# Optimization experiments

Hardware: AMD Instinct MI355X
Metric: run time of the kernel (lower is better)

The kernel has to match this reference:

```python
import jax, jax.numpy as jnp
import numpy as np
import math

D_MODEL = 2048
B, S, PAST = 4, 2048, 2048


def setup_inputs() -> dict:
    key = jax.random.key(0)
    ks = jax.random.split(key, 8)
    scale = 0.02
    x = jax.random.normal(ks[0], (B, S, D_MODEL), dtype=jnp.float32)
    past_k = jax.random.normal(ks[1], (B, PAST, D_MODEL), dtype=jnp.float32)
    past_v = jax.random.normal(ks[2], (B, PAST, D_MODEL), dtype=jnp.float32)
    Wq = jax.random.normal(ks[3], (D_MODEL, D_MODEL), dtype=jnp.float32) * scale
    Wk = jax.random.normal(ks[4], (D_MODEL, D_MODEL), dtype=jnp.float32) * scale
    Wv = jax.random.normal(ks[5], (D_MODEL, D_MODEL), dtype=jnp.float32) * scale
    Wo = jax.random.normal(ks[6], (D_MODEL, D_MODEL), dtype=jnp.float32) * scale
    bq = jnp.zeros((D_MODEL,), jnp.float32)
    bk = jnp.zeros((D_MODEL,), jnp.float32)
    bv = jnp.zeros((D_MODEL,), jnp.float32)
    bo = jnp.zeros((D_MODEL,), jnp.float32)
    return {"x": x, "past_k": past_k, "past_v": past_v,
            "Wq": Wq, "bq": bq, "Wk": Wk, "bk": bk,
            "Wv": Wv, "bv": bv, "Wo": Wo, "bo": bo}


def reference(x, past_k, past_v, Wq, bq, Wk, bk, Wv, bv, Wo, bo):
    d_model = x.shape[-1]
    # torch Linear: y = x @ W.T + b; here W is stored [out, in] equivalently square
    q = jnp.einsum('bsd,ed->bse', x, Wq) + bq
    k = jnp.einsum('bsd,ed->bse', x, Wk) + bk
    v = jnp.einsum('bsd,ed->bse', x, Wv) + bv
    k_cache = jnp.concatenate([past_k, k], axis=1)  # [B, PAST+S, D]
    v_cache = jnp.concatenate([past_v, v], axis=1)
    scores = jnp.einsum('bqd,bkd->bqk', q, k_cache) / math.sqrt(d_model)
    weights = jax.nn.softmax(scores, axis=-1)
    attn = jnp.einsum('bqk,bkd->bqd', weights, v_cache)
    out = jnp.einsum('bqd,ed->bqe', attn, Wo) + bo
    return out, (k_cache, v_cache)
```

## Files before the change

### kernel.cpp

```cpp
#include <hip/hip_runtime.h>
#include <math.h>

typedef unsigned short u16;
typedef __bf16 bf16x8 __attribute__((ext_vector_type(8)));
typedef float f32x4 __attribute__((ext_vector_type(4)));
typedef float f32x16 __attribute__((ext_vector_type(16)));
typedef short s16x8 __attribute__((ext_vector_type(8)));

#define DM 2048
#define NB 4
#define SEQ 2048
#define PAST_N 2048
#define CS 4096

__device__ __forceinline__ u16 f2bf(float f) {
  unsigned u = __float_as_uint(f);
  u += 0x7fff + ((u >> 16) & 1);
  return (u16)(u >> 16);
}
__device__ __forceinline__ float bf2f(u16 h) {
  return __uint_as_float(((unsigned)h) << 16);
}

__device__ __forceinline__ void gl_lds16(const u16* g, u16* l) {
  __builtin_amdgcn_global_load_lds(
      (const __attribute__((address_space(1))) unsigned*)g,
      (__attribute__((address_space(3))) unsigned*)l, 16, 0, 0);
}

__device__ __forceinline__ bf16x8 ldsfrag32(const u16* s, int row, int ks, int hk) {
  const int byte_off = (row * 128 + ks * 32 + hk * 16) ^ ((row & 7) << 4);
  return *(const bf16x8*)((const char*)s + byte_off);
}

__device__ __forceinline__ void stage4(const u16* __restrict__ g, int ld,
                                       u16* lwb, int t) {
#pragma unroll
  for (int j = 0; j < 4; ++j) {
    const int c = j * 512 + t;
    const int row = c >> 3;
    const int slot = (c & 7) ^ (row & 7);
    gl_lds16(g + (long)row * ld + slot * 8, lwb + j * 4096);
  }
}

template <int EPI, bool REMAP>
__global__ __launch_bounds__(512, 2) void gemm256(
    const u16* __restrict__ A, const u16* __restrict__ B,
    float* __restrict__ Cf, u16* __restrict__ Cb, const float* __restrict__ bias,
    int K, int lda, int ldb, int ldc, long strA, long strB, long strC,
    float scale) {
  __shared__ __align__(16) u16 shA[2][256 * 64];
  __shared__ __align__(16) u16 shB[2][256 * 64];
  const int t = threadIdx.x;
  const int lane = t & 63;
  const int w = t >> 6;
  const int wr = w >> 2, wc = w & 3;
  const int l31 = lane & 31, hk = lane >> 5;

  const int gx = gridDim.x, gy = gridDim.y;
  const int nwg = gx * gy * gridDim.z;
  const int orig = blockIdx.x + gx * (blockIdx.y + gy * blockIdx.z);
  const int swz = (orig & 7) * (nwg >> 3) + (orig >> 3);
  const int bx = swz % gx;
  const int r1 = swz / gx;
  const int by = r1 % gy;
  const long bz = r1 / gy;
  const int brow = by * 256, bcol = bx * 256;

  const u16* Ab = A + bz * strA + (long)brow * lda;
  const u16* Bb = B + bz * strB + (long)bcol * ldb;

  stage4(Ab, lda, &shA[0][w * 512], t);
  stage4(Bb, ldb, &shB[0][w * 512], t);

  f32x16 acc[4][2] = {};
  bf16x8 a[2][4], b[2][4];
  const int NT = K >> 6;

  for (int tt = 0; tt < NT; ++tt) {
    const int cur = tt & 1;
    asm volatile("s_waitcnt vmcnt(0)" ::: "memory");
    __builtin_amdgcn_s_barrier();
    __builtin_amdgcn_sched_barrier(0);
    if (tt + 1 < NT) {
      const int ko = (tt + 1) << 6;
      stage4(Ab + ko, lda, &shA[cur ^ 1][w * 512], t);
      stage4(Bb + ko, ldb, &shB[cur ^ 1][w * 512], t);
    }
    const u16* sA = shA[cur];
    const u16* sB = shB[cur];

#pragma unroll
    for (int mi = 0; mi < 2; ++mi)
#pragma unroll
      for (int ks = 0; ks < 4; ++ks)
        a[mi][ks] = ldsfrag32(sA, wr * 128 + mi * 32 + l31, ks, hk);
#pragma unroll
    for (int nt = 0; nt < 2; ++nt)
#pragma unroll
      for (int ks = 0; ks < 4; ++ks)
        b[nt][ks] = ldsfrag32(sB, wc * 64 + nt * 32 + l31, ks, hk);

    __builtin_amdgcn_s_setprio(1);
#pragma unroll
    for (int mi = 0; mi < 2; ++mi)
#pragma unroll
      for (int ks = 0; ks < 4; ++ks)
#pragma unroll
        for (int nt = 0; nt < 2; ++nt)
          acc[mi][nt] = __builtin_amdgcn_mfma_f32_32x32x16_bf16(
              a[mi][ks], b[ks ? nt : nt][ks], acc[mi][nt], 0, 0, 0);
    __builtin_amdgcn_s_setprio(0);

#pragma unroll
    for (int mi = 0; mi < 2; ++mi)
#pragma unroll
      for (int ks = 0; ks < 4; ++ks)
        a[mi][ks] = ldsfrag32(sA, wr * 128 + (2 + mi) * 32 + l31, ks, hk);

    __builtin_amdgcn_s_setprio(1);
#pragma unroll
    for (int mi = 0; mi < 2; ++mi)
#pragma unroll
      for (int ks = 0; ks < 4; ++ks)
#pragma unroll
        for (int nt = 0; nt < 2; ++nt)
          acc[2 + mi][nt] = __builtin_amdgcn_mfma_f32_32x32x16_bf16(
              a[mi][ks], b[nt][ks], acc[2 + mi][nt], 0, 0, 0);
    __builtin_amdgcn_s_setprio(0);
  }

  const long cb = bz * strC;
#pragma unroll
  for (int mi = 0; mi < 4; ++mi) {
#pragma unroll
    for (int nt = 0; nt < 2; ++nt) {
      const int c = bcol + wc * 64 + nt * 32 + l31;
      const float bv = bias ? bias[c] : 0.0f;
#pragma unroll
      for (int r = 0; r < 16; ++r) {
        const int row = brow + wr * 128 + mi * 32 + 8 * (r >> 2) + 4 * hk + (r & 3);
        const long orow = REMAP ? (long)((row >> 11) * CS + PAST_N + (row & (SEQ - 1)))
                                : (long)row;
        const float val = (acc[mi][nt][r] + bv) * scale;
        if (EPI == 0 || EPI == 2) Cf[cb + orow * (long)ldc + c] = val;
        if (EPI == 1 || EPI == 2) Cb[cb + orow * (long)ldc + c] = f2bf(val);
      }
    }
  }
}

__global__ __launch_bounds__(256) void cast_bf16_kn(const float* __restrict__ in,
                                                    u16* __restrict__ out) {
  const int i = blockIdx.x * 256 + threadIdx.x;
  const float4 v = ((const float4*)in)[i];
  ushort4 o;
  o.x = f2bf(v.x); o.y = f2bf(v.y); o.z = f2bf(v.z); o.w = f2bf(v.w);
  ((ushort4*)out)[i] = o;
}

__global__ __launch_bounds__(256) void copy_past_kv(const float* __restrict__ pk,
                                                    const float* __restrict__ pv,
                                                    float* __restrict__ kc,
                                                    float* __restrict__ vc,
                                                    u16* __restrict__ kb) {
  const int i = blockIdx.x * 256 + threadIdx.x;
  const int d4 = DM / 4;
  const int row = i / d4;
  const int col = i - row * d4;
  const int bb = row >> 11, p = row & (PAST_N - 1);
  const long o = ((long)(bb * CS + p)) * d4 + col;
  if (blockIdx.z == 0) {
    const float4 v = ((const float4*)pk)[i];
    ((float4*)kc)[o] = v;
    ushort4 u;
    u.x = f2bf(v.x); u.y = f2bf(v.y); u.z = f2bf(v.z); u.w = f2bf(v.w);
    ((ushort4*)kb)[o] = u;
  } else {
    ((float4*)vc)[o] = ((const float4*)pv)[i];
  }
}

__global__ __launch_bounds__(256) void transpose_cast(const float* __restrict__ vcache,
                                                      u16* __restrict__ vt) {
  __shared__ float tile[32][33];
  const int bb = blockIdx.z;
  const int k0 = blockIdx.x * 32, d0 = blockIdx.y * 32;
  const int tx = threadIdx.x & 31, ty = threadIdx.x >> 5;
  const float* src = vcache + (long)bb * CS * DM;
#pragma unroll
  for (int j = 0; j < 4; ++j)
    tile[ty + 8 * j][tx] = src[(long)(k0 + ty + 8 * j) * DM + d0 + tx];
  __syncthreads();
  u16* dst = vt + (long)bb * DM * CS;
#pragma unroll
  for (int j = 0; j < 4; ++j)
    dst[(long)(d0 + ty + 8 * j) * CS + k0 + tx] = f2bf(tile[tx][ty + 8 * j]);
}

__global__ __launch_bounds__(256) void softmax_rows(u16* __restrict__ s) {
  const long row = blockIdx.x;
  u16* p = s + row * CS;
  const int t = threadIdx.x;
  const int lane = t & 63, w = t >> 6;
  float v[16];
  s16x8 c0 = ((const s16x8*)p)[t * 2];
  s16x8 c1 = ((const s16x8*)p)[t * 2 + 1];
#pragma unroll
  for (int i = 0; i < 8; ++i) {
    v[i] = bf2f((u16)c0[i]);
    v[8 + i] = bf2f((u16)c1[i]);
  }
  float m = v[0];
#pragma unroll
  for (int i = 1; i < 16; ++i) m = fmaxf(m, v[i]);
#pragma unroll
  for (int o = 32; o >= 1; o >>= 1) m = fmaxf(m, __shfl_xor(m, o, 64));
  __shared__ float red[4];
  if (lane == 0) red[w] = m;
  __syncthreads();
  m = fmaxf(fmaxf(red[0], red[1]), fmaxf(red[2], red[3]));
  float sum = 0.f;
#pragma unroll
  for (int i = 0; i < 16; ++i) {
    v[i] = __expf(v[i] - m);
    sum += v[i];
  }
#pragma unroll
  for (int o = 32; o >= 1; o >>= 1) sum += __shfl_xor(sum, o, 64);
  __syncthreads();
  if (lane == 0) red[w] = sum;
  __syncthreads();
  sum = red[0] + red[1] + red[2] + red[3];
  const float inv = 1.0f / sum;
#pragma unroll
  for (int i = 0; i < 8; ++i) {
    c0[i] = (short)f2bf(v[i] * inv);
    c1[i] = (short)f2bf(v[8 + i] * inv);
  }
  ((s16x8*)p)[t * 2] = c0;
  ((s16x8*)p)[t * 2 + 1] = c1;
}

extern "C" void kernel_launch(void* const* d_in, const int* in_sizes, int n_in,
                              void* d_out, int out_size, void* d_ws, size_t ws_size,
                              hipStream_t stream) {
  const float* x  = (const float*)d_in[0];
  const float* pk = (const float*)d_in[1];
  const float* pv = (const float*)d_in[2];
  const float* Wq = (const float*)d_in[3];
  const float* bq = (const float*)d_in[4];
  const float* Wk = (const float*)d_in[5];
  const float* bk = (const float*)d_in[6];
  const float* Wv = (const float*)d_in[7];
  const float* bv = (const float*)d_in[8];
  const float* Wo = (const float*)d_in[9];
  const float* bo = (const float*)d_in[10];

  float* out = (float*)d_out;
  float* kc = out + (long)NB * SEQ * DM;
  float* vc = kc + (long)NB * CS * DM;

  u16* ws = (u16*)d_ws;
  u16* xb  = ws;
  u16* wqb = ws + 16777216;
  u16* wkb = wqb + 4194304;
  u16* wvb = wkb + 4194304;
  u16* wob = wvb + 4194304;
  u16* qb  = ws + 33554432;
  u16* kb  = ws + 50331648;
  u16* vtb = ws + 83886080;
  u16* sc  = ws + 117440512;

  const float qscale = 0.022097086912079608f;

  cast_bf16_kn<<<16384, 256, 0, stream>>>(x, xb);
  cast_bf16_kn<<<4096, 256, 0, stream>>>(Wq, wqb);
  cast_bf16_kn<<<4096, 256, 0, stream>>>(Wk, wkb);
  cast_bf16_kn<<<4096, 256, 0, stream>>>(Wv, wvb);
  cast_bf16_kn<<<4096, 256, 0, stream>>>(Wo, wob);

  gemm256<1, false><<<dim3(8, 32, 1), 512, 0, stream>>>(
      xb, wqb, nullptr, qb, bq, 2048, 2048, 2048, 2048, 0, 0, 0, qscale);
  gemm256<2, true><<<dim3(8, 32, 1), 512, 0, stream>>>(
      xb, wkb, kc, kb, bk, 2048, 2048, 2048, 2048, 0, 0, 0, 1.0f);
  gemm256<0, true><<<dim3(8, 32, 1), 512, 0, stream>>>(
      xb, wvb, vc, nullptr, bv, 2048, 2048, 2048, 2048, 0, 0, 0, 1.0f);

  copy_past_kv<<<dim3(16384, 1, 2), 256, 0, stream>>>(pk, pv, kc, vc, kb);

  transpose_cast<<<dim3(128, 64, 4), 256, 0, stream>>>(vc, vtb);

  gemm256<1, false><<<dim3(16, 8, 4), 512, 0, stream>>>(
      qb, kb, nullptr, sc, nullptr, 2048, 2048, 2048, 4096,
      2048L * 2048, 4096L * 2048, 2048L * 4096, 1.0f);

  softmax_rows<<<8192, 256, 0, stream>>>(sc);

  gemm256<1, false><<<dim3(8, 8, 4), 512, 0, stream>>>(
      sc, vtb, nullptr, xb, nullptr, 4096, 4096, 4096, 2048,
      2048L * 4096, 2048L * 4096, 2048L * 2048, 1.0f);

  gemm256<0, false><<<dim3(8, 32, 1), 512, 0, stream>>>(
      xb, wob, out, nullptr, bo, 2048, 2048, 2048, 2048, 0, 0, 0, 1.0f);
}
```

Measured before the change: 794.5 us.

## Switch GEMM to 16x16x32 MFMA with triple-buffered K=32 LDS pipeline

Reworks the 256x256 GEMM main loop. It uses 16x16x32 bf16 MFMA tiles instead of 32x32x16, and K-steps of 32 with a three-slot LDS ring that prefetches two tiles ahead. The LDS layout becomes fragment-native: each 16-row by 32-k block is stored so each lane reads one contiguous 16-byte vector, with no XOR swizzle. Global-to-LDS staging for A and B is split between the two MFMA phases, and the loop has more barriers and partial vmcnt waits. This is meant to overlap memory latency better, at the cost of more synchronisation per K element and possible LDS bank conflicts in the unswizzled layout.

```diff
diff --git a/kernel.cpp b/kernel.cpp
--- a/kernel.cpp
+++ b/kernel.cpp
@@ -4,7 +4,6 @@
 typedef unsigned short u16;
 typedef __bf16 bf16x8 __attribute__((ext_vector_type(8)));
 typedef float f32x4 __attribute__((ext_vector_type(4)));
-typedef float f32x16 __attribute__((ext_vector_type(16)));
 typedef short s16x8 __attribute__((ext_vector_type(8)));
 
 #define DM 2048
@@ -28,19 +27,12 @@
       (__attribute__((address_space(3))) unsigned*)l, 16, 0, 0);
 }
 
-__device__ __forceinline__ bf16x8 ldsfrag32(const u16* s, int row, int ks, int hk) {
-  const int byte_off = (row * 128 + ks * 32 + hk * 16) ^ ((row & 7) << 4);
-  return *(const bf16x8*)((const char*)s + byte_off);
-}
-
-__device__ __forceinline__ void stage4(const u16* __restrict__ g, int ld,
-                                       u16* lwb, int t) {
-#pragma unroll
-  for (int j = 0; j < 4; ++j) {
-    const int c = j * 512 + t;
-    const int row = c >> 3;
-    const int slot = (c & 7) ^ (row & 7);
-    gl_lds16(g + (long)row * ld + slot * 8, lwb + j * 4096);
+__device__ __forceinline__ void stage_op(const u16* __restrict__ g, int ld,
+                                         int ko, u16* sl, int w, int lr, int kh) {
+#pragma unroll
+  for (int j = 0; j < 2; ++j) {
+    const int u = w * 2 + j;
+    gl_lds16(g + (long)(u * 16 + lr) * ld + ko + kh * 8, sl + u * 512);
   }
 }
 
@@ -50,13 +42,13 @@
     float* __restrict__ Cf, u16* __restrict__ Cb, const float* __restrict__ bias,
     int K, int lda, int ldb, int ldc, long strA, long strB, long strC,
     float scale) {
-  __shared__ __align__(16) u16 shA[2][256 * 64];
-  __shared__ __align__(16) u16 shB[2][256 * 64];
+  __shared__ __align__(16) u16 shA[3][256 * 32];
+  __shared__ __align__(16) u16 shB[3][256 * 32];
   const int t = threadIdx.x;
   const int lane = t & 63;
   const int w = t >> 6;
   const int wr = w >> 2, wc = w & 3;
-  const int l31 = lane & 31, hk = lane >> 5;
+  const int lr = lane & 15, kh = lane >> 4;
 
   const int gx = gridDim.x, gy = gridDim.y;
   const int nwg = gx * gy * gridDim.z;
@@ -71,79 +63,83 @@
   const u16* Ab = A + bz * strA + (long)brow * lda;
   const u16* Bb = B + bz * strB + (long)bcol * ldb;
 
-  stage4(Ab, lda, &shA[0][w * 512], t);
-  stage4(Bb, ldb, &shB[0][w * 512], t);
-
-  f32x16 acc[4][2] = {};
-  bf16x8 a[2][4], b[2][4];
-  const int NT = K >> 6;
+  const int NT = K >> 5;
+
+  stage_op(Ab, lda, 0, shA[0], w, lr, kh);
+  stage_op(Bb, ldb, 0, shB[0], w, lr, kh);
+  if (NT > 1) {
+    stage_op(Ab, lda, 32, shA[1], w, lr, kh);
+    stage_op(Bb, ldb, 32, shB[1], w, lr, kh);
+  }
+
+  f32x4 acc[8][4] = {};
+  bf16x8 a[4], b[4];
 
   for (int tt = 0; tt < NT; ++tt) {
-    const int cur = tt & 1;
-    asm volatile("s_waitcnt vmcnt(0)" ::: "memory");
+    const int slot = tt % 3;
+    const u16* sA = shA[slot];
+    const u16* sB = shB[slot];
+    const int ns = (tt + 2) % 3;
+    const bool st = (tt + 2 < NT);
+    const int ko = (tt + 2) << 5;
+
+    if (tt + 1 < NT)
+      asm volatile("s_waitcnt vmcnt(4)" ::: "memory");
+    else
+      asm volatile("s_waitcnt vmcnt(0)" ::: "memory");
     __builtin_amdgcn_s_barrier();
     __builtin_amdgcn_sched_barrier(0);
-    if (tt + 1 < NT) {
-      const int ko = (tt + 1) << 6;
-      stage4(Ab + ko, lda, &shA[cur ^ 1][w * 512], t);
-      stage4(Bb + ko, ldb, &shB[cur ^ 1][w * 512], t);
-    }
-    const u16* sA = shA[cur];
-    const u16* sB = shB[cur];
-
-#pragma unroll
-    for (int mi = 0; mi < 2; ++mi)
-#pragma unroll
-      for (int ks = 0; ks < 4; ++ks)
-        a[mi][ks] = ldsfrag32(sA, wr * 128 + mi * 32 + l31, ks, hk);
-#pragma unroll
-    for (int nt = 0; nt < 2; ++nt)
-#pragma unroll
-      for (int ks = 0; ks < 4; ++ks)
-        b[nt][ks] = ldsfrag32(sB, wc * 64 + nt * 32 + l31, ks, hk);
-
+
+#pragma unroll
+    for (int mi = 0; mi < 4; ++mi)
+      a[mi] = *(const bf16x8*)(sA + (wr * 8 + mi) * 512 + lane * 8);
+#pragma unroll
+    for (int ni = 0; ni < 4; ++ni)
+      b[ni] = *(const bf16x8*)(sB + (wc * 4 + ni) * 512 + lane * 8);
+    if (st) stage_op(Ab, lda, ko, shA[ns], w, lr, kh);
+    __builtin_amdgcn_s_barrier();
+    asm volatile("s_waitcnt lgkmcnt(0)" ::: "memory");
+    __builtin_amdgcn_sched_barrier(0);
     __builtin_amdgcn_s_setprio(1);
 #pragma unroll
-    for (int mi = 0; mi < 2; ++mi)
-#pragma unroll
-      for (int ks = 0; ks < 4; ++ks)
-#pragma unroll
-        for (int nt = 0; nt < 2; ++nt)
-          acc[mi][nt] = __builtin_amdgcn_mfma_f32_32x32x16_bf16(
-              a[mi][ks], b[ks ? nt : nt][ks], acc[mi][nt], 0, 0, 0);
+    for (int mi = 0; mi < 4; ++mi)
+#pragma unroll
+      for (int ni = 0; ni < 4; ++ni)
+        acc[mi][ni] = __builtin_amdgcn_mfma_f32_16x16x32_bf16(
+            a[mi], b[ni], acc[mi][ni], 0, 0, 0);
     __builtin_amdgcn_s_setprio(0);
-
-#pragma unroll
-    for (int mi = 0; mi < 2; ++mi)
-#pragma unroll
-      for (int ks = 0; ks < 4; ++ks)
-        a[mi][ks] = ldsfrag32(sA, wr * 128 + (2 + mi) * 32 + l31, ks, hk);
-
+    __builtin_amdgcn_s_barrier();
+
+#pragma unroll
+    for (int mi = 0; mi < 4; ++mi)
+      a[mi] = *(const bf16x8*)(sA + (wr * 8 + 4 + mi) * 512 + lane * 8);
+    if (st) stage_op(Bb, ldb, ko, shB[ns], w, lr, kh);
+    asm volatile("s_waitcnt lgkmcnt(0)" ::: "memory");
+    __builtin_amdgcn_sched_barrier(0);
     __builtin_amdgcn_s_setprio(1);
 #pragma unroll
-    for (int mi = 0; mi < 2; ++mi)
-#pragma unroll
-      for (int ks = 0; ks < 4; ++ks)
-#pragma unroll
-        for (int nt = 0; nt < 2; ++nt)
-          acc[2 + mi][nt] = __builtin_amdgcn_mfma_f32_32x32x16_bf16(
-              a[mi][ks], b[nt][ks], acc[2 + mi][nt], 0, 0, 0);
+    for (int mi = 0; mi < 4; ++mi)
+#pragma unroll
+      for (int ni = 0; ni < 4; ++ni)
+        acc[4 + mi][ni] = __builtin_amdgcn_mfma_f32_16x16x32_bf16(
+            a[mi], b[ni], acc[4 + mi][ni], 0, 0, 0);
     __builtin_amdgcn_s_setprio(0);
   }
 
   const long cb = bz * strC;
 #pragma unroll
-  for (int mi = 0; mi < 4; ++mi) {
-#pragma unroll
-    for (int nt = 0; nt < 2; ++nt) {
-      const int c = bcol + wc * 64 + nt * 32 + l31;
+  for (int mi = 0; mi < 8; ++mi) {
+    const int r0 = wr * 128 + mi * 16 + kh * 4;
+#pragma unroll
+    for (int ni = 0; ni < 4; ++ni) {
+      const int c = bcol + wc * 64 + ni * 16 + lr;
       const float bv = bias ? bias[c] : 0.0f;
 #pragma unroll
-      for (int r = 0; r < 16; ++r) {
-        const int row = brow + wr * 128 + mi * 32 + 8 * (r >> 2) + 4 * hk + (r & 3);
+      for (int r = 0; r < 4; ++r) {
+        const int row = brow + r0 + r;
         const long orow = REMAP ? (long)((row >> 11) * CS + PAST_N + (row & (SEQ - 1)))
                                 : (long)row;
-        const float val = (acc[mi][nt][r] + bv) * scale;
+        const float val = (acc[mi][ni][r] + bv) * scale;
         if (EPI == 0 || EPI == 2) Cf[cb + orow * (long)ldc + c] = val;
         if (EPI == 1 || EPI == 2) Cb[cb + orow * (long)ldc + c] = f2bf(val);
       }
```

After: 819.9 us. 1.03x slower.
